# Performance work log

Measured on AMD Instinct MI355X. Metric: run time of the kernel, lower is better.

## Reference

```python
import jax, jax.numpy as jnp
import numpy as np

N_NODES = 100000
N_EDGES = 1600000
IN_F = 128
HID = 128
OUT_F = 40


def _gcn_conv(x, W, b, src, dst):
    # PyG GCNConv: h = x @ W; out[dst] += norm * h[src]; out += b
    n = x.shape[0]
    h = x @ W  # [N, out_channels]
    deg = jnp.zeros((n,), h.dtype).at[dst].add(jnp.ones((dst.shape[0],), h.dtype))
    dinv = jnp.where(deg > 0, jax.lax.rsqrt(deg), 0.0)  # deg^{-1/2}
    norm = dinv[src] * dinv[dst]  # [E+N]
    msg = h[src] * norm[:, None]  # [E+N, out_channels] gather
    out = jnp.zeros_like(h).at[dst].add(msg)  # scatter-add at targets
    if b is not None:
        out = out + b
    return out


def setup_inputs() -> dict:
    key = jax.random.key(0)
    k_x, k_e, k1, k2, k3, kb1, kb2 = jax.random.split(key, 7)
    x = jax.random.normal(k_x, (N_NODES, IN_F), dtype=jnp.float32)
    edge_index = jax.random.randint(k_e, (2, N_EDGES), 0, N_NODES, dtype=jnp.int64)
    s_in = 1.0 / np.sqrt(IN_F)
    s_h = 1.0 / np.sqrt(HID)
    W_in = jax.random.normal(k1, (IN_F, HID), dtype=jnp.float32) * s_in
    b_in = jnp.zeros((HID,), dtype=jnp.float32)
    W_mid = jax.random.normal(k2, (HID, HID), dtype=jnp.float32) * s_h
    b_mid = jnp.zeros((HID,), dtype=jnp.float32)
    W_out = jax.random.normal(k3, (HID, OUT_F), dtype=jnp.float32) * s_h
    return {"x": x, "edge_index": edge_index, "W_in": W_in, "b_in": b_in,
            "W_mid": W_mid, "b_mid": b_mid, "W_out": W_out}


def reference(x, edge_index, W_in, b_in, W_mid, b_mid, W_out):
    n = x.shape[0]
    loops = jnp.arange(n, dtype=edge_index.dtype)
    src = jnp.concatenate([edge_index[0], loops])  # add self-loops
    dst = jnp.concatenate([edge_index[1], loops])
    h = jax.nn.relu(_gcn_conv(x, W_in, b_in, src, dst))
    h = jax.nn.relu(_gcn_conv(h, W_mid, b_mid, src, dst))
    h = _gcn_conv(h, W_out, None, src, dst)  # out_conv: bias=False
    return jax.nn.log_softmax(h, axis=1)
```

## Files before the change

### kernel.cpp

```cpp
#include <hip/hip_runtime.h>
#include <math.h>

#define N_NODES 100000
#define N_EDGES 1600000
#define NBUCK 391
#define BSTRIDE 4608

typedef __attribute__((ext_vector_type(8))) _Float16 h8v;
typedef __attribute__((ext_vector_type(4))) float f32x4;
typedef __attribute__((ext_vector_type(2))) int i32x2;


__launch_bounds__(256)
__global__ void k_prep(const int* __restrict__ srcv, const int* __restrict__ dstv,
                       int* __restrict__ bcnt, unsigned int* __restrict__ ebuf,
                       const float* __restrict__ W1, const float* __restrict__ W2,
                       const float* __restrict__ W3, _Float16* __restrict__ Wt,
                       _Float16* __restrict__ bufA, _Float16* __restrict__ zbuf) {
    const int tid = threadIdx.x;
    const int bid = blockIdx.x;

    if (bid >= 391) {
        if (bid == 543) {
            if (tid < 128) bufA[(size_t)N_NODES * 128 + tid] = (_Float16)0.f;
            if (tid < 64)  zbuf[(size_t)N_NODES * 64 + tid] = (_Float16)0.f;
            return;
        }
        int idx = (bid - 391) * 256 + tid;
        if (idx >= 304 * 128) return;
        int n = idx / 128, k = idx % 128;
        const float* W;
        int ncols, nloc;
        _Float16 *ph, *pl;
        if (n < 128)      { W = W1; ncols = 128; nloc = n;       ph = Wt;                 pl = Wt + 128 * 128; }
        else if (n < 256) { W = W2; ncols = 128; nloc = n - 128; ph = Wt + 2 * 128 * 128; pl = Wt + 3 * 128 * 128; }
        else              { W = W3; ncols = 40;  nloc = n - 256; ph = Wt + 4 * 128 * 128; pl = Wt + 4 * 128 * 128 + 48 * 128; }
        float v = (nloc < ncols) ? W[k * ncols + nloc] : 0.f;
        _Float16 hi = (_Float16)v;
        _Float16 lo = (_Float16)(v - (float)hi);
        ph[nloc * 128 + k] = hi;
        pl[nloc * 128 + k] = lo;
        return;
    }

    __shared__ int hist[NBUCK];
    __shared__ int cur[NBUCK];
    for (int t = tid; t < NBUCK; t += 256) hist[t] = 0;
    __syncthreads();
    const int base = bid * 4096;
#pragma unroll
    for (int i = 0; i < 16; i++) {
        int e = base + i * 256 + tid;
        if (e < N_EDGES) atomicAdd(&hist[dstv[e] >> 8], 1);
    }
    __syncthreads();
    for (int t = tid; t < NBUCK; t += 256)
        if (hist[t]) cur[t] = t * BSTRIDE + atomicAdd(&bcnt[t], hist[t]);
    __syncthreads();
#pragma unroll
    for (int i = 0; i < 16; i++) {
        int e = base + i * 256 + tid;
        if (e < N_EDGES) {
            int d = dstv[e];
            int p = atomicAdd(&cur[d >> 8], 1);
            ebuf[p] = ((unsigned int)srcv[e] << 8) | (unsigned int)(d & 255);
        }
    }
}

__launch_bounds__(256)
__global__ void k_bucket(const unsigned int* __restrict__ ebuf, const int* __restrict__ bcnt,
                         i32x2* __restrict__ rowse, float* __restrict__ dinv,
                         int* __restrict__ colidx) {
    __shared__ int cnt[256];
    __shared__ int s[256];
    __shared__ int cur[256];
    const int tid = threadIdx.x;
    const int b = blockIdx.x;
    const int e0 = b * BSTRIDE;
    const int e1 = e0 + bcnt[b];
    cnt[tid] = 0;
    __syncthreads();
    for (int e = e0 + tid; e < e1; e += 256) atomicAdd(&cnt[ebuf[e] & 255u], 1);
    __syncthreads();
    int v = cnt[tid];
    int x = v;
    s[tid] = x;
    __syncthreads();
    for (int d = 1; d < 256; d <<= 1) {
        int t = (tid >= d) ? s[tid - d] : 0;
        __syncthreads();
        x += t;
        s[tid] = x;
        __syncthreads();
    }
    int start = e0 + x - v;
    int node = b * 256 + tid;
    if (node < N_NODES) {
        i32x2 se;
        se.x = start;
        se.y = start + v;
        rowse[node] = se;
        dinv[node] = rsqrtf((float)(v + 1));
    }
    cur[tid] = start;
    __syncthreads();
    for (int e = e0 + tid; e < e1; e += 256) {
        unsigned int sd = ebuf[e];
        int pos = atomicAdd(&cur[sd & 255u], 1);
        colidx[pos] = (int)(sd >> 8);
    }
}


#define GEMM_GRID 625
#define NTILES 3125

__launch_bounds__(256, 2)
__global__ void k_gemm128_f32(const float* __restrict__ Af,
                              const _Float16* __restrict__ Wthi, const _Float16* __restrict__ Wtlo,
                              const float* __restrict__ dinv, _Float16* __restrict__ out) {
    const int lane = threadIdx.x & 63;
    const int wi = threadIdx.x >> 6;
    const int nb = wi * 32;
    const int nn = lane & 15;
    const int kq = (lane >> 4) * 8;
    const int quad = lane >> 4;

    h8v bh[4][2], bl[4][2];
#pragma unroll
    for (int c = 0; c < 4; c++)
#pragma unroll
        for (int t = 0; t < 2; t++) {
            int off = (nb + t * 16 + nn) * 128 + c * 32 + kq;
            bh[c][t] = *(const h8v*)(Wthi + off);
            bl[c][t] = *(const h8v*)(Wtlo + off);
        }

    for (int rt = blockIdx.x; rt < NTILES; rt += GEMM_GRID) {
        const int r0 = rt * 32;
        f32x4 acc[2][2] = {};
#pragma unroll
        for (int c = 0; c < 4; c++) {
            h8v a[2];
#pragma unroll
            for (int m = 0; m < 2; m++) {
                const float* p = Af + (size_t)(r0 + m * 16 + nn) * 128 + c * 32 + kq;
                float4 p0 = *(const float4*)p;
                float4 p1 = *(const float4*)(p + 4);
                h8v av = {(_Float16)p0.x, (_Float16)p0.y, (_Float16)p0.z, (_Float16)p0.w,
                          (_Float16)p1.x, (_Float16)p1.y, (_Float16)p1.z, (_Float16)p1.w};
                a[m] = av;
            }
#pragma unroll
            for (int m = 0; m < 2; m++)
#pragma unroll
                for (int t = 0; t < 2; t++) {
                    acc[m][t] = __builtin_amdgcn_mfma_f32_16x16x32_f16(a[m], bh[c][t], acc[m][t], 0, 0, 0);
                    acc[m][t] = __builtin_amdgcn_mfma_f32_16x16x32_f16(a[m], bl[c][t], acc[m][t], 0, 0, 0);
                }
        }
#pragma unroll
        for (int m = 0; m < 2; m++)
#pragma unroll
            for (int reg = 0; reg < 4; reg++) {
                int r = r0 + m * 16 + quad * 4 + reg;
                float dv = dinv[r];
#pragma unroll
                for (int t = 0; t < 2; t++)
                    __builtin_nontemporal_store((_Float16)(acc[m][t][reg] * dv),
                                                out + (size_t)r * 128 + nb + t * 16 + nn);
            }
    }
}

__launch_bounds__(256, 2)
__global__ void k_gemm128(const _Float16* __restrict__ A,
                          const _Float16* __restrict__ Wthi, const _Float16* __restrict__ Wtlo,
                          const float* __restrict__ dinv, _Float16* __restrict__ out) {
    const int lane = threadIdx.x & 63;
    const int wi = threadIdx.x >> 6;
    const int nb = wi * 32;
    const int nn = lane & 15;
    const int kq = (lane >> 4) * 8;
    const int quad = lane >> 4;

    h8v bh[4][2], bl[4][2];
#pragma unroll
    for (int c = 0; c < 4; c++)
#pragma unroll
        for (int t = 0; t < 2; t++) {
            int off = (nb + t * 16 + nn) * 128 + c * 32 + kq;
            bh[c][t] = *(const h8v*)(Wthi + off);
            bl[c][t] = *(const h8v*)(Wtlo + off);
        }

    for (int rt = blockIdx.x; rt < NTILES; rt += GEMM_GRID) {
        const int r0 = rt * 32;
        f32x4 acc[2][2] = {};
#pragma unroll
        for (int c = 0; c < 4; c++) {
            h8v a[2];
#pragma unroll
            for (int m = 0; m < 2; m++)
                a[m] = *(const h8v*)(A + (size_t)(r0 + m * 16 + nn) * 128 + c * 32 + kq);
#pragma unroll
            for (int m = 0; m < 2; m++)
#pragma unroll
                for (int t = 0; t < 2; t++) {
                    acc[m][t] = __builtin_amdgcn_mfma_f32_16x16x32_f16(a[m], bh[c][t], acc[m][t], 0, 0, 0);
                    acc[m][t] = __builtin_amdgcn_mfma_f32_16x16x32_f16(a[m], bl[c][t], acc[m][t], 0, 0, 0);
                }
        }
#pragma unroll
        for (int m = 0; m < 2; m++)
#pragma unroll
            for (int reg = 0; reg < 4; reg++) {
                int r = r0 + m * 16 + quad * 4 + reg;
                float dv = dinv[r];
#pragma unroll
                for (int t = 0; t < 2; t++)
                    __builtin_nontemporal_store((_Float16)(acc[m][t][reg] * dv),
                                                out + (size_t)r * 128 + nb + t * 16 + nn);
            }
    }
}

#define G40_GRID 160

__launch_bounds__(256, 2)
__global__ void k_gemm40(const _Float16* __restrict__ A,
                         const _Float16* __restrict__ Wthi, const _Float16* __restrict__ Wtlo,
                         const float* __restrict__ dinv, _Float16* __restrict__ out) {
    const int lane = threadIdx.x & 63;
    const int wi = threadIdx.x >> 6;
    const int nn = lane & 15;
    const int kq = (lane >> 4) * 8;
    const int quad = lane >> 4;

    h8v bh[4][3], bl[4][3];
#pragma unroll
    for (int c = 0; c < 4; c++)
#pragma unroll
        for (int t = 0; t < 3; t++) {
            int off = (t * 16 + nn) * 128 + c * 32 + kq;
            bh[c][t] = *(const h8v*)(Wthi + off);
            bl[c][t] = *(const h8v*)(Wtlo + off);
        }

    for (int rt = blockIdx.x * 4 + wi; rt < NTILES; rt += G40_GRID * 4) {
        const int r0 = rt * 32;
        f32x4 acc[2][3] = {};
#pragma unroll
        for (int c = 0; c < 4; c++) {
            h8v a[2];
#pragma unroll
            for (int m = 0; m < 2; m++)
                a[m] = *(const h8v*)(A + (size_t)(r0 + m * 16 + nn) * 128 + c * 32 + kq);
#pragma unroll
            for (int m = 0; m < 2; m++)
#pragma unroll
                for (int t = 0; t < 3; t++) {
                    acc[m][t] = __builtin_amdgcn_mfma_f32_16x16x32_f16(a[m], bh[c][t], acc[m][t], 0, 0, 0);
                    acc[m][t] = __builtin_amdgcn_mfma_f32_16x16x32_f16(a[m], bl[c][t], acc[m][t], 0, 0, 0);
                }
        }
#pragma unroll
        for (int m = 0; m < 2; m++)
#pragma unroll
            for (int reg = 0; reg < 4; reg++) {
                int r = r0 + m * 16 + quad * 4 + reg;
                float dv = dinv[r];
#pragma unroll
                for (int t = 0; t < 3; t++)
                    __builtin_nontemporal_store((_Float16)(acc[m][t][reg] * dv),
                                                out + (size_t)r * 64 + t * 16 + nn);
            }
    }
}


__launch_bounds__(256)
__global__ void k_agg4(const _Float16* __restrict__ hp, const i32x2* __restrict__ rowse,
                       const int* __restrict__ colidx, const float* __restrict__ bias,
                       _Float16* __restrict__ outp) {
    const int lane = threadIdx.x & 63;
    const int wid = (blockIdx.x * blockDim.x + threadIdx.x) >> 6;
    const int rs = lane >> 4;
    const int cp = lane & 15;
    const int r = wid * 4 + rs;

    const i32x2 se = __builtin_nontemporal_load(rowse + r);
    const int deg = se.y - se.x;
    int m = deg;
    m = max(m, __shfl_xor(m, 16));
    m = max(m, __shfl_xor(m, 32));

    const _Float16* hpc = hp + cp * 8;
    h8v acc = {};
    for (int it = 0; it < m; it += 4) {
        int i0 = se.x + it;
        int s0 = __builtin_nontemporal_load(colidx + i0);
        int s1 = __builtin_nontemporal_load(colidx + i0 + 1);
        int s2 = __builtin_nontemporal_load(colidx + i0 + 2);
        int s3 = __builtin_nontemporal_load(colidx + i0 + 3);
        s0 = (it < deg) ? s0 : N_NODES;
        s1 = (it + 1 < deg) ? s1 : N_NODES;
        s2 = (it + 2 < deg) ? s2 : N_NODES;
        s3 = (it + 3 < deg) ? s3 : N_NODES;
        h8v v0 = *(const h8v*)(hpc + (size_t)s0 * 128);
        h8v v1 = *(const h8v*)(hpc + (size_t)s1 * 128);
        h8v v2 = *(const h8v*)(hpc + (size_t)s2 * 128);
        h8v v3 = *(const h8v*)(hpc + (size_t)s3 * 128);
        acc += v0;
        acc += v1;
        acc += v2;
        acc += v3;
    }

    h8v sv = *(const h8v*)(hpc + (size_t)r * 128);
    float dv = rsqrtf((float)(deg + 1));
    const float* bp = bias + cp * 8;
    float4 b0 = *(const float4*)bp;
    float4 b1 = *(const float4*)(bp + 4);
    float bb[8] = {b0.x, b0.y, b0.z, b0.w, b1.x, b1.y, b1.z, b1.w};
    h8v o;
#pragma unroll
    for (int j = 0; j < 8; j++) {
        float s = (float)acc[j] + (float)sv[j];
        o[j] = (_Float16)fmaxf(fmaf(dv, s, bb[j]), 0.f);
    }
    __builtin_nontemporal_store(o, (h8v*)(outp + (size_t)r * 128 + cp * 8));
}


__launch_bounds__(256)
__global__ void k_agg_out(const _Float16* __restrict__ hp, const i32x2* __restrict__ rowse,
                          const int* __restrict__ colidx, float* __restrict__ out) {
    const int lane = threadIdx.x & 63;
    const int wid = (blockIdx.x * blockDim.x + threadIdx.x) >> 6;
    const int rs = lane >> 3;
    const int cp = lane & 7;
    const int r = wid * 8 + rs;

    const i32x2 se = __builtin_nontemporal_load(rowse + r);
    const int deg = se.y - se.x;
    int m = deg;
    m = max(m, __shfl_xor(m, 8));
    m = max(m, __shfl_xor(m, 16));
    m = max(m, __shfl_xor(m, 32));

    const _Float16* hpc = hp + cp * 8;
    h8v acc = {};
    for (int it = 0; it < m; it += 4) {
        int i0 = se.x + it;
        int s0 = __builtin_nontemporal_load(colidx + i0);
        int s1 = __builtin_nontemporal_load(colidx + i0 + 1);
        int s2 = __builtin_nontemporal_load(colidx + i0 + 2);
        int s3 = __builtin_nontemporal_load(colidx + i0 + 3);
        s0 = (it < deg) ? s0 : N_NODES;
        s1 = (it + 1 < deg) ? s1 : N_NODES;
        s2 = (it + 2 < deg) ? s2 : N_NODES;
        s3 = (it + 3 < deg) ? s3 : N_NODES;
        h8v v0 = *(const h8v*)(hpc + (size_t)s0 * 64);
        h8v v1 = *(const h8v*)(hpc + (size_t)s1 * 64);
        h8v v2 = *(const h8v*)(hpc + (size_t)s2 * 64);
        h8v v3 = *(const h8v*)(hpc + (size_t)s3 * 64);
        acc += v0;
        acc += v1;
        acc += v2;
        acc += v3;
    }

    h8v sv = *(const h8v*)(hpc + (size_t)r * 64);
    float dv = rsqrtf((float)(deg + 1));
    float z[8];
#pragma unroll
    for (int j = 0; j < 8; j++) z[j] = dv * ((float)acc[j] + (float)sv[j]);

    const bool act = cp < 5;
    float pm = -INFINITY;
    if (act) {
#pragma unroll
        for (int j = 0; j < 8; j++) pm = fmaxf(pm, z[j]);
    }
    pm = fmaxf(pm, __shfl_xor(pm, 1));
    pm = fmaxf(pm, __shfl_xor(pm, 2));
    pm = fmaxf(pm, __shfl_xor(pm, 4));
    float pe = 0.f;
    if (act) {
#pragma unroll
        for (int j = 0; j < 8; j++) pe += __expf(z[j] - pm);
    }
    pe += __shfl_xor(pe, 1);
    pe += __shfl_xor(pe, 2);
    pe += __shfl_xor(pe, 4);
    float lse = __logf(pe);
    if (act) {
        float* po = out + (size_t)r * 40 + cp * 8;
        f32x4 o0 = {z[0] - pm - lse, z[1] - pm - lse, z[2] - pm - lse, z[3] - pm - lse};
        f32x4 o1 = {z[4] - pm - lse, z[5] - pm - lse, z[6] - pm - lse, z[7] - pm - lse};
        __builtin_nontemporal_store(o0, (f32x4*)po);
        __builtin_nontemporal_store(o1, (f32x4*)(po + 4));
    }
}


extern "C" void kernel_launch(void* const* d_in, const int* in_sizes, int n_in,
                              void* d_out, int out_size, void* d_ws, size_t ws_size,
                              hipStream_t stream) {
    const float* x     = (const float*)d_in[0];
    const int*   ei    = (const int*)d_in[1];
    const float* W_in  = (const float*)d_in[2];
    const float* b_in  = (const float*)d_in[3];
    const float* W_mid = (const float*)d_in[4];
    const float* b_mid = (const float*)d_in[5];
    const float* W_out = (const float*)d_in[6];
    float* out = (float*)d_out;

    const int* srcv = ei;
    const int* dstv = ei + N_EDGES;

    char* w = (char*)d_ws;
    float* dinv   = (float*)(w);
    i32x2* rowse  = (i32x2*)(w + (1ull << 19));
    int* bcnt     = (int*)(w + 1507328);
    int* colidx   = (int*)(w + (2ull << 20));
    unsigned int* ebuf = (unsigned int*)(w + (10ull << 20));
    _Float16* Wt  = (_Float16*)(w + (18ull << 20));
    _Float16* bufA = (_Float16*)(w + (19ull << 20));
    _Float16* bufB = (_Float16*)(w + (45ull << 20));
    _Float16* zbuf = (_Float16*)(w + (71ull << 20));

    _Float16* W1h = Wt;
    _Float16* W1l = Wt + 128 * 128;
    _Float16* W2h = Wt + 2 * 128 * 128;
    _Float16* W2l = Wt + 3 * 128 * 128;
    _Float16* W3h = Wt + 4 * 128 * 128;
    _Float16* W3l = Wt + 4 * 128 * 128 + 48 * 128;

    (void)hipMemsetAsync(bcnt, 0, NBUCK * sizeof(int), stream);
    k_prep<<<544, 256, 0, stream>>>(srcv, dstv, bcnt, ebuf, W_in, W_mid, W_out, Wt, bufA, zbuf);
    k_bucket<<<NBUCK, 256, 0, stream>>>(ebuf, bcnt, rowse, dinv, colidx);

    const int AGG4_BLOCKS = N_NODES / 16;
    const int AGGO_BLOCKS = N_NODES / 32;

    k_gemm128_f32<<<GEMM_GRID, 256, 0, stream>>>(x, W1h, W1l, dinv, bufA);
    k_agg4<<<AGG4_BLOCKS, 256, 0, stream>>>(bufA, rowse, colidx, b_in, bufB);
    k_gemm128<<<GEMM_GRID, 256, 0, stream>>>(bufB, W2h, W2l, dinv, bufA);
    k_agg4<<<AGG4_BLOCKS, 256, 0, stream>>>(bufA, rowse, colidx, b_mid, bufB);
    k_gemm40<<<G40_GRID, 256, 0, stream>>>(bufB, W3h, W3l, dinv, zbuf);
    k_agg_out<<<AGGO_BLOCKS, 256, 0, stream>>>(zbuf, rowse, colidx, out);
}
```

Baseline: 388.0 us.

## Fuse neighbor aggregation with following GEMM via shared-memory tile

Merges each aggregation kernel with the next layer's GEMM. A block aggregates 32 rows into an XOR-swizzled LDS tile, then runs MFMA on it, so the intermediate aggregated features never go through global memory. This cuts two kernel launches and one full write-plus-read of a 100k×128 fp16 buffer per layer. It also swaps nontemporal loads and stores for normal ones so gathered rows can stay cached. In exchange, the GEMM weights now stay in registers while irregular gathers run, which may hurt occupancy, and the GEMM phase waits on the slowest row in each block.

```diff
diff --git a/kernel.cpp b/kernel.cpp
--- a/kernel.cpp
+++ b/kernel.cpp
@@ -16,13 +16,17 @@
                        int* __restrict__ bcnt, unsigned int* __restrict__ ebuf,
                        const float* __restrict__ W1, const float* __restrict__ W2,
                        const float* __restrict__ W3, _Float16* __restrict__ Wt,
-                       _Float16* __restrict__ bufA, _Float16* __restrict__ zbuf) {
+                       _Float16* __restrict__ bufA, _Float16* __restrict__ bufB,
+                       _Float16* __restrict__ zbuf) {
     const int tid = threadIdx.x;
     const int bid = blockIdx.x;
 
     if (bid >= 391) {
         if (bid == 543) {
-            if (tid < 128) bufA[(size_t)N_NODES * 128 + tid] = (_Float16)0.f;
+            if (tid < 128) {
+                bufA[(size_t)N_NODES * 128 + tid] = (_Float16)0.f;
+                bufB[(size_t)N_NODES * 128 + tid] = (_Float16)0.f;
+            }
             if (tid < 64)  zbuf[(size_t)N_NODES * 64 + tid] = (_Float16)0.f;
             return;
         }
@@ -168,22 +172,25 @@
                 float dv = dinv[r];
 #pragma unroll
                 for (int t = 0; t < 2; t++)
-                    __builtin_nontemporal_store((_Float16)(acc[m][t][reg] * dv),
-                                                out + (size_t)r * 128 + nb + t * 16 + nn);
-            }
-    }
-}
+                    out[(size_t)r * 128 + nb + t * 16 + nn] = (_Float16)(acc[m][t][reg] * dv);
+            }
+    }
+}
+
 
 __launch_bounds__(256, 2)
-__global__ void k_gemm128(const _Float16* __restrict__ A,
-                          const _Float16* __restrict__ Wthi, const _Float16* __restrict__ Wtlo,
-                          const float* __restrict__ dinv, _Float16* __restrict__ out) {
+__global__ void k_fused128(const _Float16* __restrict__ hp, const i32x2* __restrict__ rowse,
+                           const int* __restrict__ colidx, const float* __restrict__ bias,
+                           const float* __restrict__ dinv,
+                           const _Float16* __restrict__ Wthi, const _Float16* __restrict__ Wtlo,
+                           _Float16* __restrict__ out) {
+    __shared__ __align__(16) _Float16 As[32 * 128];
     const int lane = threadIdx.x & 63;
     const int wi = threadIdx.x >> 6;
+    const int nn = lane & 15;
+    const int quad = lane >> 4;
+    const int kq = quad * 8;
     const int nb = wi * 32;
-    const int nn = lane & 15;
-    const int kq = (lane >> 4) * 8;
-    const int quad = lane >> 4;
 
     h8v bh[4][2], bl[4][2];
 #pragma unroll
@@ -195,142 +202,185 @@
             bl[c][t] = *(const h8v*)(Wtlo + off);
         }
 
-    for (int rt = blockIdx.x; rt < NTILES; rt += GEMM_GRID) {
-        const int r0 = rt * 32;
-        f32x4 acc[2][2] = {};
-#pragma unroll
-        for (int c = 0; c < 4; c++) {
-            h8v a[2];
-#pragma unroll
-            for (int m = 0; m < 2; m++)
-                a[m] = *(const h8v*)(A + (size_t)(r0 + m * 16 + nn) * 128 + c * 32 + kq);
-#pragma unroll
-            for (int m = 0; m < 2; m++)
-#pragma unroll
-                for (int t = 0; t < 2; t++) {
-                    acc[m][t] = __builtin_amdgcn_mfma_f32_16x16x32_f16(a[m], bh[c][t], acc[m][t], 0, 0, 0);
-                    acc[m][t] = __builtin_amdgcn_mfma_f32_16x16x32_f16(a[m], bl[c][t], acc[m][t], 0, 0, 0);
-                }
-        }
-#pragma unroll
-        for (int m = 0; m < 2; m++)
-#pragma unroll
-            for (int reg = 0; reg < 4; reg++) {
-                int r = r0 + m * 16 + quad * 4 + reg;
-                float dv = dinv[r];
-#pragma unroll
-                for (int t = 0; t < 2; t++)
-                    __builtin_nontemporal_store((_Float16)(acc[m][t][reg] * dv),
-                                                out + (size_t)r * 128 + nb + t * 16 + nn);
-            }
-    }
-}
-
-#define G40_GRID 160
-
-__launch_bounds__(256, 2)
-__global__ void k_gemm40(const _Float16* __restrict__ A,
-                         const _Float16* __restrict__ Wthi, const _Float16* __restrict__ Wtlo,
-                         const float* __restrict__ dinv, _Float16* __restrict__ out) {
-    const int lane = threadIdx.x & 63;
-    const int wi = threadIdx.x >> 6;
-    const int nn = lane & 15;
-    const int kq = (lane >> 4) * 8;
-    const int quad = lane >> 4;
-
-    h8v bh[4][3], bl[4][3];
-#pragma unroll
-    for (int c = 0; c < 4; c++)
-#pragma unroll
-        for (int t = 0; t < 3; t++) {
-            int off = (t * 16 + nn) * 128 + c * 32 + kq;
-            bh[c][t] = *(const h8v*)(Wthi + off);
-            bl[c][t] = *(const h8v*)(Wtlo + off);
-        }
-
-    for (int rt = blockIdx.x * 4 + wi; rt < NTILES; rt += G40_GRID * 4) {
-        const int r0 = rt * 32;
-        f32x4 acc[2][3] = {};
-#pragma unroll
-        for (int c = 0; c < 4; c++) {
-            h8v a[2];
-#pragma unroll
-            for (int m = 0; m < 2; m++)
-                a[m] = *(const h8v*)(A + (size_t)(r0 + m * 16 + nn) * 128 + c * 32 + kq);
-#pragma unroll
-            for (int m = 0; m < 2; m++)
-#pragma unroll
-                for (int t = 0; t < 3; t++) {
-                    acc[m][t] = __builtin_amdgcn_mfma_f32_16x16x32_f16(a[m], bh[c][t], acc[m][t], 0, 0, 0);
-                    acc[m][t] = __builtin_amdgcn_mfma_f32_16x16x32_f16(a[m], bl[c][t], acc[m][t], 0, 0, 0);
-                }
-        }
-#pragma unroll
-        for (int m = 0; m < 2; m++)
-#pragma unroll
-            for (int reg = 0; reg < 4; reg++) {
-                int r = r0 + m * 16 + quad * 4 + reg;
-                float dv = dinv[r];
-#pragma unroll
-                for (int t = 0; t < 3; t++)
-                    __builtin_nontemporal_store((_Float16)(acc[m][t][reg] * dv),
-                                                out + (size_t)r * 64 + t * 16 + nn);
-            }
-    }
-}
-
-
-__launch_bounds__(256)
-__global__ void k_agg4(const _Float16* __restrict__ hp, const i32x2* __restrict__ rowse,
-                       const int* __restrict__ colidx, const float* __restrict__ bias,
-                       _Float16* __restrict__ outp) {
-    const int lane = threadIdx.x & 63;
-    const int wid = (blockIdx.x * blockDim.x + threadIdx.x) >> 6;
-    const int rs = lane >> 4;
-    const int cp = lane & 15;
-    const int r = wid * 4 + rs;
-
-    const i32x2 se = __builtin_nontemporal_load(rowse + r);
-    const int deg = se.y - se.x;
-    int m = deg;
-    m = max(m, __shfl_xor(m, 16));
-    m = max(m, __shfl_xor(m, 32));
-
+    const int r0 = blockIdx.x * 32;
+
+    const int rs = quad;
+    const int cp = nn;
     const _Float16* hpc = hp + cp * 8;
-    h8v acc = {};
-    for (int it = 0; it < m; it += 4) {
-        int i0 = se.x + it;
-        int s0 = __builtin_nontemporal_load(colidx + i0);
-        int s1 = __builtin_nontemporal_load(colidx + i0 + 1);
-        int s2 = __builtin_nontemporal_load(colidx + i0 + 2);
-        int s3 = __builtin_nontemporal_load(colidx + i0 + 3);
-        s0 = (it < deg) ? s0 : N_NODES;
-        s1 = (it + 1 < deg) ? s1 : N_NODES;
-        s2 = (it + 2 < deg) ? s2 : N_NODES;
-        s3 = (it + 3 < deg) ? s3 : N_NODES;
-        h8v v0 = *(const h8v*)(hpc + (size_t)s0 * 128);
-        h8v v1 = *(const h8v*)(hpc + (size_t)s1 * 128);
-        h8v v2 = *(const h8v*)(hpc + (size_t)s2 * 128);
-        h8v v3 = *(const h8v*)(hpc + (size_t)s3 * 128);
-        acc += v0;
-        acc += v1;
-        acc += v2;
-        acc += v3;
-    }
-
-    h8v sv = *(const h8v*)(hpc + (size_t)r * 128);
-    float dv = rsqrtf((float)(deg + 1));
     const float* bp = bias + cp * 8;
     float4 b0 = *(const float4*)bp;
     float4 b1 = *(const float4*)(bp + 4);
     float bb[8] = {b0.x, b0.y, b0.z, b0.w, b1.x, b1.y, b1.z, b1.w};
-    h8v o;
-#pragma unroll
-    for (int j = 0; j < 8; j++) {
-        float s = (float)acc[j] + (float)sv[j];
-        o[j] = (_Float16)fmaxf(fmaf(dv, s, bb[j]), 0.f);
-    }
-    __builtin_nontemporal_store(o, (h8v*)(outp + (size_t)r * 128 + cp * 8));
+#pragma unroll
+    for (int p = 0; p < 2; p++) {
+        const int rl = wi * 8 + p * 4 + rs;
+        const int r = r0 + rl;
+        const i32x2 se = rowse[r];
+        const int deg = se.y - se.x;
+        int m = deg;
+        m = max(m, __shfl_xor(m, 16));
+        m = max(m, __shfl_xor(m, 32));
+        h8v acc = {};
+        for (int it = 0; it < m; it += 4) {
+            int i0 = se.x + it;
+            int s0 = colidx[i0];
+            int s1 = colidx[i0 + 1];
+            int s2 = colidx[i0 + 2];
+            int s3 = colidx[i0 + 3];
+            s0 = (it < deg) ? s0 : N_NODES;
+            s1 = (it + 1 < deg) ? s1 : N_NODES;
+            s2 = (it + 2 < deg) ? s2 : N_NODES;
+            s3 = (it + 3 < deg) ? s3 : N_NODES;
+            h8v v0 = *(const h8v*)(hpc + (size_t)s0 * 128);
+            h8v v1 = *(const h8v*)(hpc + (size_t)s1 * 128);
+            h8v v2 = *(const h8v*)(hpc + (size_t)s2 * 128);
+            h8v v3 = *(const h8v*)(hpc + (size_t)s3 * 128);
+            acc += v0;
+            acc += v1;
+            acc += v2;
+            acc += v3;
+        }
+        h8v sv = *(const h8v*)(hpc + (size_t)r * 128);
+        float dv = rsqrtf((float)(deg + 1));
+        h8v o;
+#pragma unroll
+        for (int j = 0; j < 8; j++) {
+            float sx = (float)acc[j] + (float)sv[j];
+            o[j] = (_Float16)fmaxf(fmaf(dv, sx, bb[j]), 0.f);
+        }
+        *(h8v*)(As + rl * 128 + ((cp ^ (rl & 15)) * 8)) = o;
+    }
+    __syncthreads();
+
+    f32x4 acc2[2][2] = {};
+#pragma unroll
+    for (int c = 0; c < 4; c++) {
+        h8v a[2];
+#pragma unroll
+        for (int mm = 0; mm < 2; mm++) {
+            int R = mm * 16 + nn;
+            int ch = (c * 4 + quad) ^ (R & 15);
+            a[mm] = *(const h8v*)(As + R * 128 + ch * 8);
+        }
+#pragma unroll
+        for (int mm = 0; mm < 2; mm++)
+#pragma unroll
+            for (int t = 0; t < 2; t++) {
+                acc2[mm][t] = __builtin_amdgcn_mfma_f32_16x16x32_f16(a[mm], bh[c][t], acc2[mm][t], 0, 0, 0);
+                acc2[mm][t] = __builtin_amdgcn_mfma_f32_16x16x32_f16(a[mm], bl[c][t], acc2[mm][t], 0, 0, 0);
+            }
+    }
+#pragma unroll
+    for (int mm = 0; mm < 2; mm++)
+#pragma unroll
+        for (int reg = 0; reg < 4; reg++) {
+            int r = r0 + mm * 16 + quad * 4 + reg;
+            float dv = dinv[r];
+#pragma unroll
+            for (int t = 0; t < 2; t++)
+                out[(size_t)r * 128 + nb + t * 16 + nn] = (_Float16)(acc2[mm][t][reg] * dv);
+        }
+}
+
+__launch_bounds__(256, 2)
+__global__ void k_fused40(const _Float16* __restrict__ hp, const i32x2* __restrict__ rowse,
+                          const int* __restrict__ colidx, const float* __restrict__ bias,
+                          const float* __restrict__ dinv,
+                          const _Float16* __restrict__ Wthi, const _Float16* __restrict__ Wtlo,
+                          _Float16* __restrict__ out) {
+    __shared__ __align__(16) _Float16 As[32 * 128];
+    const int lane = threadIdx.x & 63;
+    const int wi = threadIdx.x >> 6;
+    const int nn = lane & 15;
+    const int quad = lane >> 4;
+    const int kq = quad * 8;
+
+    h8v bh[4], bl[4];
+    if (wi < 3) {
+#pragma unroll
+        for (int c = 0; c < 4; c++) {
+            int off = (wi * 16 + nn) * 128 + c * 32 + kq;
+            bh[c] = *(const h8v*)(Wthi + off);
+            bl[c] = *(const h8v*)(Wtlo + off);
+        }
+    }
+
+    const int r0 = blockIdx.x * 32;
+
+    const int rs = quad;
+    const int cp = nn;
+    const _Float16* hpc = hp + cp * 8;
+    const float* bp = bias + cp * 8;
+    float4 b0 = *(const float4*)bp;
+    float4 b1 = *(const float4*)(bp + 4);
+    float bb[8] = {b0.x, b0.y, b0.z, b0.w, b1.x, b1.y, b1.z, b1.w};
+#pragma unroll
+    for (int p = 0; p < 2; p++) {
+        const int rl = wi * 8 + p * 4 + rs;
+        const int r = r0 + rl;
+        const i32x2 se = rowse[r];
+        const int deg = se.y - se.x;
+        int m = deg;
+        m = max(m, __shfl_xor(m, 16));
+        m = max(m, __shfl_xor(m, 32));
+        h8v acc = {};
+        for (int it = 0; it < m; it += 4) {
+            int i0 = se.x + it;
+            int s0 = colidx[i0];
+            int s1 = colidx[i0 + 1];
+            int s2 = colidx[i0 + 2];
+            int s3 = colidx[i0 + 3];
+            s0 = (it < deg) ? s0 : N_NODES;
+            s1 = (it + 1 < deg) ? s1 : N_NODES;
+            s2 = (it + 2 < deg) ? s2 : N_NODES;
+            s3 = (it + 3 < deg) ? s3 : N_NODES;
+            h8v v0 = *(const h8v*)(hpc + (size_t)s0 * 128);
+            h8v v1 = *(const h8v*)(hpc + (size_t)s1 * 128);
+            h8v v2 = *(const h8v*)(hpc + (size_t)s2 * 128);
+            h8v v3 = *(const h8v*)(hpc + (size_t)s3 * 128);
+            acc += v0;
+            acc += v1;
+            acc += v2;
+            acc += v3;
+        }
+        h8v sv = *(const h8v*)(hpc + (size_t)r * 128);
+        float dv = rsqrtf((float)(deg + 1));
+        h8v o;
+#pragma unroll
+        for (int j = 0; j < 8; j++) {
+            float sx = (float)acc[j] + (float)sv[j];
+            o[j] = (_Float16)fmaxf(fmaf(dv, sx, bb[j]), 0.f);
+        }
+        *(h8v*)(As + rl * 128 + ((cp ^ (rl & 15)) * 8)) = o;
+    }
+    __syncthreads();
+
+    if (wi < 3) {
+        f32x4 acc2[2] = {};
+#pragma unroll
+        for (int c = 0; c < 4; c++) {
+            h8v a[2];
+#pragma unroll
+            for (int mm = 0; mm < 2; mm++) {
+                int R = mm * 16 + nn;
+                int ch = (c * 4 + quad) ^ (R & 15);
+                a[mm] = *(const h8v*)(As + R * 128 + ch * 8);
+            }
+#pragma unroll
+            for (int mm = 0; mm < 2; mm++) {
+                acc2[mm] = __builtin_amdgcn_mfma_f32_16x16x32_f16(a[mm], bh[c], acc2[mm], 0, 0, 0);
+                acc2[mm] = __builtin_amdgcn_mfma_f32_16x16x32_f16(a[mm], bl[c], acc2[mm], 0, 0, 0);
+            }
+        }
+#pragma unroll
+        for (int mm = 0; mm < 2; mm++)
+#pragma unroll
+            for (int reg = 0; reg < 4; reg++) {
+                int r = r0 + mm * 16 + quad * 4 + reg;
+                float dv = dinv[r];
+                out[(size_t)r * 64 + wi * 16 + nn] = (_Float16)(acc2[mm][reg] * dv);
+            }
+    }
 }
 
 
@@ -343,7 +393,7 @@
     const int cp = lane & 7;
     const int r = wid * 8 + rs;
 
-    const i32x2 se = __builtin_nontemporal_load(rowse + r);
+    const i32x2 se = rowse[r];
     const int deg = se.y - se.x;
     int m = deg;
     m = max(m, __shfl_xor(m, 8));
@@ -354,10 +404,10 @@
     h8v acc = {};
     for (int it = 0; it < m; it += 4) {
         int i0 = se.x + it;
-        int s0 = __builtin_nontemporal_load(colidx + i0);
-        int s1 = __builtin_nontemporal_load(colidx + i0 + 1);
-        int s2 = __builtin_nontemporal_load(colidx + i0 + 2);
-        int s3 = __builtin_nontemporal_load(colidx + i0 + 3);
+        int s0 = colidx[i0];
+        int s1 = colidx[i0 + 1];
+        int s2 = colidx[i0 + 2];
+        int s3 = colidx[i0 + 3];
         s0 = (it < deg) ? s0 : N_NODES;
         s1 = (it + 1 < deg) ? s1 : N_NODES;
         s2 = (it + 2 < deg) ? s2 : N_NODES;
@@ -398,10 +448,10 @@
     float lse = __logf(pe);
     if (act) {
         float* po = out + (size_t)r * 40 + cp * 8;
-        f32x4 o0 = {z[0] - pm - lse, z[1] - pm - lse, z[2] - pm - lse, z[3] - pm - lse};
-        f32x4 o1 = {z[4] - pm - lse, z[5] - pm - lse, z[6] - pm - lse, z[7] - pm - lse};
-        __builtin_nontemporal_store(o0, (f32x4*)po);
-        __builtin_nontemporal_store(o1, (f32x4*)(po + 4));
+        float4 o0 = make_float4(z[0] - pm - lse, z[1] - pm - lse, z[2] - pm - lse, z[3] - pm - lse);
+        float4 o1 = make_float4(z[4] - pm - lse, z[5] - pm - lse, z[6] - pm - lse, z[7] - pm - lse);
+        *(float4*)po = o0;
+        *(float4*)(po + 4) = o1;
     }
 }
 
@@ -440,16 +490,11 @@
     _Float16* W3l = Wt + 4 * 128 * 128 + 48 * 128;
 
     (void)hipMemsetAsync(bcnt, 0, NBUCK * sizeof(int), stream);
-    k_prep<<<544, 256, 0, stream>>>(srcv, dstv, bcnt, ebuf, W_in, W_mid, W_out, Wt, bufA, zbuf);
+    k_prep<<<544, 256, 0, stream>>>(srcv, dstv, bcnt, ebuf, W_in, W_mid, W_out, Wt, bufA, bufB, zbuf);
     k_bucket<<<NBUCK, 256, 0, stream>>>(ebuf, bcnt, rowse, dinv, colidx);
 
-    const int AGG4_BLOCKS = N_NODES / 16;
-    const int AGGO_BLOCKS = N_NODES / 32;
-
     k_gemm128_f32<<<GEMM_GRID, 256, 0, stream>>>(x, W1h, W1l, dinv, bufA);
-    k_agg4<<<AGG4_BLOCKS, 256, 0, stream>>>(bufA, rowse, colidx, b_in, bufB);
-    k_gemm128<<<GEMM_GRID, 256, 0, stream>>>(bufB, W2h, W2l, dinv, bufA);
-    k_agg4<<<AGG4_BLOCKS, 256, 0, stream>>>(bufA, rowse, colidx, b_mid, bufB);
-    k_gemm40<<<G40_GRID, 256, 0, stream>>>(bufB, W3h, W3l, dinv, zbuf);
-    k_agg_out<<<AGGO_BLOCKS, 256, 0, stream>>>(zbuf, rowse, colidx, out);
-}
+    k_fused128<<<NTILES, 256, 0, stream>>>(bufA, rowse, colidx, b_in, dinv, W2h, W2l, bufB);
+    k_fused40<<<NTILES, 256, 0, stream>>>(bufB, rowse, colidx, b_mid, dinv, W3h, W3l, zbuf);
+    k_agg_out<<<N_NODES / 32, 256, 0, stream>>>(zbuf, rowse, colidx, out);
+}
```

New measurement: 353.0 us. 1.1x faster.
